# Kernel optimization log

Hardware: AMD Instinct MI355X
Metric: run time of the kernel (lower is better)

The kernel has to match this reference:

```python
import jax, jax.numpy as jnp
import numpy as np

N = 30000
E_RAND = 480000
NFEAT = 512
NHID = 64
NHEADS = 8
NCLASS = 500
ALPHA = 0.2


def setup_inputs() -> dict:
    key = jax.random.key(0)
    ks = jax.random.split(key, 8)
    features = jax.random.normal(ks[0], (N, NFEAT), dtype=jnp.float32)
    src = jax.random.randint(ks[1], (E_RAND,), 0, N, dtype=jnp.int32)
    dst = jax.random.randint(ks[2], (E_RAND,), 0, N, dtype=jnp.int32)
    loop = jnp.arange(N, dtype=jnp.int32)
    edge_index = jnp.stack([jnp.concatenate([src, loop]), jnp.concatenate([dst, loop])])  # [2, E]
    # xavier-normal-ish scaling keeps exp(-leakyrelu(.)) in a sane range
    W = jax.random.normal(ks[3], (NHEADS, NFEAT, NHID), dtype=jnp.float32) * (1.414 * np.sqrt(2.0 / (NFEAT + NHID)))
    a = jax.random.normal(ks[4], (NHEADS, 2 * NHID), dtype=jnp.float32) * (1.414 * np.sqrt(2.0 / (1 + 2 * NHID)))
    out_W = jax.random.normal(ks[5], (NHID * NHEADS, NCLASS), dtype=jnp.float32) * (1.414 * np.sqrt(2.0 / (NHID * NHEADS + NCLASS)))
    out_a = jax.random.normal(ks[6], (2 * NCLASS,), dtype=jnp.float32) * (1.414 * np.sqrt(2.0 / (1 + 2 * NCLASS)))
    return {"features": features, "edge_index": edge_index, "W": W, "a": a, "out_W": out_W, "out_a": out_a}


def _sp_gat_layer(x, W, a, src, dst, concat):
    # h = x @ W  -> [N, F']
    h = x @ W
    f = h.shape[1]
    n = x.shape[0]
    # a . cat(h[src], h[dst]) == (h @ a[:f])[src] + (h @ a[f:])[dst]  (avoids [E, 2F'] concat)
    s_src = h @ a[:f]
    s_dst = h @ a[f:]
    logits = s_src[src] + s_dst[dst]                      # [E]
    edge_e = jnp.exp(-jax.nn.leaky_relu(logits, negative_slope=ALPHA))
    # special_spmm(edge, edge_e, [N,N], ones)  -> per-row sum of attention values
    e_rowsum = jax.ops.segment_sum(edge_e, src, num_segments=n)        # [N]
    # special_spmm(edge, edge_e, [N,N], h)     -> attention-weighted neighbor sum
    h_prime = jax.ops.segment_sum(edge_e[:, None] * h[dst], src, num_segments=n)  # [N, F']
    h_prime = h_prime / e_rowsum[:, None]
    return jax.nn.elu(h_prime) if concat else h_prime


def reference(features, edge_index, W, a, out_W, out_a):
    src, dst = edge_index[0], edge_index[1]
    # multi-head sparse GAT (concat=True per head), python loop over fixed small head count
    heads = [_sp_gat_layer(features, W[i], a[i], src, dst, concat=True) for i in range(W.shape[0])]
    x = jnp.concatenate(heads, axis=1)                    # [N, nhid*nheads]
    out = jax.nn.elu(_sp_gat_layer(x, out_W, out_a, src, dst, concat=False))  # [N, nclass]
    return out
```

## Files before the change

### kernel.cpp

```cpp
#include <hip/hip_runtime.h>
#include <math.h>

typedef __attribute__((ext_vector_type(8))) short short8;
typedef __attribute__((ext_vector_type(4))) float f32x4;

#define NFEAT 512
#define HID_ALL 512
#define NCLASS 500
#define ALPHA 0.2f
#define BM 128
#define BN 128

__device__ __forceinline__ ushort f32_to_bf16(float f) {
    union { float f; unsigned u; } v; v.f = f;
    unsigned u = v.u;
    unsigned r = (u + 0x7FFFu + ((u >> 16) & 1u)) >> 16;
    return (ushort)r;
}
__device__ __forceinline__ void unpack8(uint4 u, float* f) {
    f[0] = __uint_as_float(u.x << 16);
    f[1] = __uint_as_float(u.x & 0xFFFF0000u);
    f[2] = __uint_as_float(u.y << 16);
    f[3] = __uint_as_float(u.y & 0xFFFF0000u);
    f[4] = __uint_as_float(u.z << 16);
    f[5] = __uint_as_float(u.z & 0xFFFF0000u);
    f[6] = __uint_as_float(u.w << 16);
    f[7] = __uint_as_float(u.w & 0xFFFF0000u);
}
__device__ __forceinline__ float att_w(float lg) {
    return __expf(lg > 0.f ? -lg : -ALPHA * lg);
}
__device__ __forceinline__ void gload16(const void* g, void* l) {
    __builtin_amdgcn_global_load_lds(
        (const __attribute__((address_space(1))) unsigned int*)g,
        (__attribute__((address_space(3))) unsigned int*)l,
        16, 0, 0);
}

__global__ void prep_kernel(const float* __restrict__ W, ushort* __restrict__ W1T,
                            const float* __restrict__ oW, ushort* __restrict__ W2T,
                            const float* __restrict__ oa, float* __restrict__ oas,
                            float* __restrict__ oad,
                            int* __restrict__ cnt, int* __restrict__ cur,
                            float* __restrict__ s2, float* __restrict__ d2, int N) {
    int idx = blockIdx.x * blockDim.x + threadIdx.x;
    if (idx < 512 * 512) {
        int c = idx >> 9, f = idx & 511;
        int head = c >> 6, k = c & 63;
        W1T[idx] = f32_to_bf16(W[(head << 15) + (f << 6) + k]);
        float v = (c < NCLASS) ? oW[f * NCLASS + c] : 0.f;
        W2T[idx] = f32_to_bf16(v);
    }
    if (idx < 512) {
        oas[idx] = (idx < NCLASS) ? oa[idx] : 0.f;
        oad[idx] = (idx < NCLASS) ? oa[NCLASS + idx] : 0.f;
    }
    if (idx < N) { cnt[idx] = 0; cur[idx] = 0; s2[idx] = 0.f; d2[idx] = 0.f; }
}

__global__ void cast_feat_kernel(const float* __restrict__ in, ushort* __restrict__ out, int n4) {
    int stride = gridDim.x * blockDim.x;
    for (int i = blockIdx.x * blockDim.x + threadIdx.x; i < n4; i += stride) {
        float4 v = reinterpret_cast<const float4*>(in)[i];
        ushort4 o;
        o.x = f32_to_bf16(v.x); o.y = f32_to_bf16(v.y);
        o.z = f32_to_bf16(v.z); o.w = f32_to_bf16(v.w);
        reinterpret_cast<ushort4*>(out)[i] = o;
    }
}

__global__ void edge_count_kernel(const int* __restrict__ src, int* __restrict__ cnt, int E) {
    int e = blockIdx.x * blockDim.x + threadIdx.x;
    if (e < E) atomicAdd(&cnt[src[e]], 1);
}

__global__ __launch_bounds__(1024) void scan_kernel(const int* __restrict__ cnt,
                                                    int* __restrict__ rowptr, int n) {
    __shared__ int part[1024];
    int t = threadIdx.x;
    int chunk = (n + 1023) >> 10;
    int beg = t * chunk;
    int end = beg + chunk; if (end > n) end = n;
    int s = 0;
    for (int i = beg; i < end; i++) s += cnt[i];
    part[t] = s;
    __syncthreads();
    for (int off = 1; off < 1024; off <<= 1) {
        int v = part[t];
        int add = (t >= off) ? part[t - off] : 0;
        __syncthreads();
        part[t] = v + add;
        __syncthreads();
    }
    int base = (t > 0) ? part[t - 1] : 0;
    for (int i = beg; i < end; i++) { rowptr[i] = base; base += cnt[i]; }
    if (t == 1023) rowptr[n] = part[1023];
}

__global__ void scatter_kernel(const int* __restrict__ src, const int* __restrict__ dst,
                               const int* __restrict__ rowptr, int* __restrict__ cur,
                               int* __restrict__ colidx, int E) {
    int e = blockIdx.x * blockDim.x + threadIdx.x;
    if (e >= E) return;
    int s = src[e];
    int p = rowptr[s] + atomicAdd(&cur[s], 1);
    colidx[p] = dst[e];
}

template <int MODE>
__global__ __launch_bounds__(256) void gemm_fused_kernel(const ushort* __restrict__ A,
                                                         const ushort* __restrict__ Bt,
                                                         ushort* __restrict__ C,
                                                         const float* __restrict__ av,
                                                         const float* __restrict__ av2,
                                                         float* __restrict__ sv,
                                                         float* __restrict__ dv,
                                                         int M) {
    __shared__ ushort As[BM * 64];
    __shared__ ushort Bs[BN * 64];
    int m0 = blockIdx.x * BM;
    int n0 = blockIdx.y * BN;
    int t = threadIdx.x;
    int lane = t & 63, wid = t >> 6;
    int wr = wid >> 1, wc = wid & 1;
    int g = lane >> 4, r15 = lane & 15;
    int srow = lane >> 3;
    int schunk = lane & 7;
    f32x4 acc[4][4] = {};
    for (int k0 = 0; k0 < 512; k0 += 64) {
        __syncthreads();
#pragma unroll
        for (int j = 0; j < 4; j++) {
            int rb = j * 32 + wid * 8;
            int r = rb + srow;
            int ca = (schunk ^ (srow & 7)) << 3;
            int rowA = m0 + r; if (rowA >= M) rowA = M - 1;
            gload16(&A[(size_t)rowA * 512 + k0 + ca], &As[rb * 64]);
            int rowB = n0 + r;
            gload16(&Bt[(size_t)rowB * 512 + k0 + ca], &Bs[rb * 64]);
        }
        __syncthreads();
#pragma unroll
        for (int kk = 0; kk < 2; kk++) {
            int coff = ((kk * 4 + g) ^ (r15 & 7)) << 3;
            short8 af[4], bfr[4];
#pragma unroll
            for (int mi = 0; mi < 4; mi++)
                af[mi] = *reinterpret_cast<const short8*>(&As[((wr << 6) + mi * 16 + r15) * 64 + coff]);
#pragma unroll
            for (int ni = 0; ni < 4; ni++)
                bfr[ni] = *reinterpret_cast<const short8*>(&Bs[((wc << 6) + ni * 16 + r15) * 64 + coff]);
#pragma unroll
            for (int mi = 0; mi < 4; mi++)
#pragma unroll
                for (int ni = 0; ni < 4; ni++)
                    acc[mi][ni] = __builtin_amdgcn_mfma_f32_16x16x32_bf16(af[mi], bfr[ni], acc[mi][ni], 0, 0, 0);
        }
    }
    int fr = g << 2;
    int col = r15;
#pragma unroll
    for (int mi = 0; mi < 4; mi++)
#pragma unroll
        for (int ni = 0; ni < 4; ni++)
#pragma unroll
            for (int r = 0; r < 4; r++) {
                int grow = m0 + (wr << 6) + mi * 16 + fr + r;
                if (grow < M) {
                    int gcol = n0 + (wc << 6) + ni * 16 + col;
                    C[(size_t)grow * 512 + gcol] = f32_to_bf16(acc[mi][ni][r]);
                }
            }
    float ws[4], wd[4];
    int h = (n0 >> 6) + wc;
#pragma unroll
    for (int ni = 0; ni < 4; ni++) {
        if (MODE == 0) {
            int k = ni * 16 + col;
            ws[ni] = av[(h << 7) + k];
            wd[ni] = av[(h << 7) + 64 + k];
        } else {
            int gcol = n0 + (wc << 6) + ni * 16 + col;
            ws[ni] = av[gcol];
            wd[ni] = av2[gcol];
        }
    }
#pragma unroll
    for (int mi = 0; mi < 4; mi++)
#pragma unroll
        for (int r = 0; r < 4; r++) {
            float ps = 0.f, pd = 0.f;
#pragma unroll
            for (int ni = 0; ni < 4; ni++) {
                float v = acc[mi][ni][r];
                ps += v * ws[ni];
                pd += v * wd[ni];
            }
#pragma unroll
            for (int off = 1; off < 16; off <<= 1) {
                ps += __shfl_xor(ps, off);
                pd += __shfl_xor(pd, off);
            }
            int grow = m0 + (wr << 6) + mi * 16 + fr + r;
            if (col == 0 && grow < M) {
                if (MODE == 0) {
                    sv[(grow << 3) + h] = ps;
                    dv[(grow << 3) + h] = pd;
                } else {
                    atomicAdd(&sv[grow], ps);
                    atomicAdd(&dv[grow], pd);
                }
            }
        }
}

__global__ __launch_bounds__(256) void agg1_kernel(const ushort* __restrict__ h1,
                                                   const float* __restrict__ s1,
                                                   const float* __restrict__ d1,
                                                   const int* __restrict__ rowptr,
                                                   const int* __restrict__ colidx,
                                                   ushort* __restrict__ x, int N) {
    int lane = threadIdx.x & 63;
    int n = (blockIdx.x << 2) + (threadIdx.x >> 6);
    if (n >= N) return;
    int h = lane >> 3;
    float sn = s1[(n << 3) + h];
    float acc[8] = {0.f, 0.f, 0.f, 0.f, 0.f, 0.f, 0.f, 0.f};
    float rsum = 0.f;
    int beg = rowptr[n], end = rowptr[n + 1];
    int i = beg;
    for (; i + 4 <= end; i += 4) {
        int dv0 = colidx[i], dv1 = colidx[i + 1], dv2 = colidx[i + 2], dv3 = colidx[i + 3];
        float g0 = d1[(dv0 << 3) + h];
        float g1 = d1[(dv1 << 3) + h];
        float g2 = d1[(dv2 << 3) + h];
        float g3 = d1[(dv3 << 3) + h];
        uint4 u0 = *reinterpret_cast<const uint4*>(&h1[(size_t)dv0 * 512 + lane * 8]);
        uint4 u1 = *reinterpret_cast<const uint4*>(&h1[(size_t)dv1 * 512 + lane * 8]);
        uint4 u2 = *reinterpret_cast<const uint4*>(&h1[(size_t)dv2 * 512 + lane * 8]);
        uint4 u3 = *reinterpret_cast<const uint4*>(&h1[(size_t)dv3 * 512 + lane * 8]);
        float w0 = att_w(sn + g0), w1 = att_w(sn + g1), w2 = att_w(sn + g2), w3 = att_w(sn + g3);
        rsum += (w0 + w1) + (w2 + w3);
        float f[8];
        unpack8(u0, f);
#pragma unroll
        for (int q = 0; q < 8; q++) acc[q] += w0 * f[q];
        unpack8(u1, f);
#pragma unroll
        for (int q = 0; q < 8; q++) acc[q] += w1 * f[q];
        unpack8(u2, f);
#pragma unroll
        for (int q = 0; q < 8; q++) acc[q] += w2 * f[q];
        unpack8(u3, f);
#pragma unroll
        for (int q = 0; q < 8; q++) acc[q] += w3 * f[q];
    }
    for (; i < end; i++) {
        int dv = colidx[i];
        float w = att_w(sn + d1[(dv << 3) + h]);
        rsum += w;
        uint4 u = *reinterpret_cast<const uint4*>(&h1[(size_t)dv * 512 + lane * 8]);
        float f[8]; unpack8(u, f);
#pragma unroll
        for (int q = 0; q < 8; q++) acc[q] += w * f[q];
    }
    float inv = 1.f / rsum;
    uint ov[4];
#pragma unroll
    for (int p = 0; p < 4; p++) {
        float v0 = acc[2 * p] * inv;     v0 = v0 > 0.f ? v0 : __expf(v0) - 1.f;
        float v1 = acc[2 * p + 1] * inv; v1 = v1 > 0.f ? v1 : __expf(v1) - 1.f;
        ov[p] = (uint)f32_to_bf16(v0) | ((uint)f32_to_bf16(v1) << 16);
    }
    uint4 o; o.x = ov[0]; o.y = ov[1]; o.z = ov[2]; o.w = ov[3];
    *reinterpret_cast<uint4*>(&x[(size_t)n * 512 + lane * 8]) = o;
}

__global__ __launch_bounds__(256) void agg2_kernel(const ushort* __restrict__ h2,
                                                   const float* __restrict__ s2,
                                                   const float* __restrict__ d2,
                                                   const int* __restrict__ rowptr,
                                                   const int* __restrict__ colidx,
                                                   float* __restrict__ out, int N) {
    int lane = threadIdx.x & 63;
    int n = (blockIdx.x << 2) + (threadIdx.x >> 6);
    if (n >= N) return;
    int c0 = lane * 8;
    float sn = s2[n];
    float acc[8] = {0.f, 0.f, 0.f, 0.f, 0.f, 0.f, 0.f, 0.f};
    float rsum = 0.f;
    int beg = rowptr[n], end = rowptr[n + 1];
    int i = beg;
    for (; i + 4 <= end; i += 4) {
        int dv0 = colidx[i], dv1 = colidx[i + 1], dv2 = colidx[i + 2], dv3 = colidx[i + 3];
        float g0 = d2[dv0], g1 = d2[dv1], g2 = d2[dv2], g3 = d2[dv3];
        uint4 u0 = *reinterpret_cast<const uint4*>(&h2[(size_t)dv0 * 512 + c0]);
        uint4 u1 = *reinterpret_cast<const uint4*>(&h2[(size_t)dv1 * 512 + c0]);
        uint4 u2 = *reinterpret_cast<const uint4*>(&h2[(size_t)dv2 * 512 + c0]);
        uint4 u3 = *reinterpret_cast<const uint4*>(&h2[(size_t)dv3 * 512 + c0]);
        float w0 = att_w(sn + g0), w1 = att_w(sn + g1), w2 = att_w(sn + g2), w3 = att_w(sn + g3);
        rsum += (w0 + w1) + (w2 + w3);
        float f[8];
        unpack8(u0, f);
#pragma unroll
        for (int q = 0; q < 8; q++) acc[q] += w0 * f[q];
        unpack8(u1, f);
#pragma unroll
        for (int q = 0; q < 8; q++) acc[q] += w1 * f[q];
        unpack8(u2, f);
#pragma unroll
        for (int q = 0; q < 8; q++) acc[q] += w2 * f[q];
        unpack8(u3, f);
#pragma unroll
        for (int q = 0; q < 8; q++) acc[q] += w3 * f[q];
    }
    for (; i < end; i++) {
        int dv = colidx[i];
        float w = att_w(sn + d2[dv]);
        rsum += w;
        uint4 u = *reinterpret_cast<const uint4*>(&h2[(size_t)dv * 512 + c0]);
        float f[8]; unpack8(u, f);
#pragma unroll
        for (int q = 0; q < 8; q++) acc[q] += w * f[q];
    }
    float inv = 1.f / rsum;
#pragma unroll
    for (int q = 0; q < 8; q++) {
        int c = c0 + q;
        if (c < NCLASS) {
            float v = acc[q] * inv;
            v = v > 0.f ? v : __expf(v) - 1.f;
            out[(size_t)n * NCLASS + c] = v;
        }
    }
}

extern "C" void kernel_launch(void* const* d_in, const int* in_sizes, int n_in,
                              void* d_out, int out_size, void* d_ws, size_t ws_size,
                              hipStream_t stream) {
    const float* features = (const float*)d_in[0];
    const int* edge_index = (const int*)d_in[1];
    const float* W = (const float*)d_in[2];
    const float* a = (const float*)d_in[3];
    const float* out_W = (const float*)d_in[4];
    const float* out_a = (const float*)d_in[5];
    float* out = (float*)d_out;

    int N = in_sizes[0] / NFEAT;
    int E = in_sizes[1] / 2;
    const int* src = edge_index;
    const int* dst = edge_index + E;

    char* base = (char*)d_ws;
    size_t off = 0;
    auto alloc = [&](size_t bytes) -> char* {
        char* r = base + off;
        off += (bytes + 255) & ~(size_t)255;
        return r;
    };
    ushort* featb = (ushort*)alloc((size_t)N * 512 * 2);
    ushort* h1b   = (ushort*)alloc((size_t)N * 512 * 2);
    ushort* xb    = (ushort*)alloc((size_t)N * 512 * 2);
    ushort* h2b   = featb;
    ushort* w1t   = (ushort*)alloc(512 * 512 * 2);
    ushort* w2t   = (ushort*)alloc(512 * 512 * 2);
    float* s1 = (float*)alloc((size_t)N * 8 * 4);
    float* d1 = (float*)alloc((size_t)N * 8 * 4);
    float* s2 = (float*)alloc((size_t)N * 4);
    float* d2 = (float*)alloc((size_t)N * 4);
    float* oas = (float*)alloc(512 * 4);
    float* oad = (float*)alloc(512 * 4);
    int* rowptr = (int*)alloc((size_t)(N + 1) * 4);
    int* colidx = (int*)alloc((size_t)E * 4);
    int* cnt = (int*)alloc((size_t)N * 4);
    int* cur = (int*)alloc((size_t)N * 4);
    if (off > ws_size) return;

    prep_kernel<<<1024, 256, 0, stream>>>(W, w1t, out_W, w2t, out_a, oas, oad, cnt, cur, s2, d2, N);
    cast_feat_kernel<<<2048, 256, 0, stream>>>(features, featb, N * 512 / 4);
    edge_count_kernel<<<(E + 255) / 256, 256, 0, stream>>>(src, cnt, E);
    scan_kernel<<<1, 1024, 0, stream>>>(cnt, rowptr, N);
    scatter_kernel<<<(E + 255) / 256, 256, 0, stream>>>(src, dst, rowptr, cur, colidx, E);

    dim3 gemm_grid((N + BM - 1) / BM, HID_ALL / BN);
    gemm_fused_kernel<0><<<gemm_grid, 256, 0, stream>>>(featb, w1t, h1b, a, nullptr, s1, d1, N);
    agg1_kernel<<<(N + 3) / 4, 256, 0, stream>>>(h1b, s1, d1, rowptr, colidx, xb, N);
    gemm_fused_kernel<1><<<gemm_grid, 256, 0, stream>>>(xb, w2t, h2b, oas, oad, s2, d2, N);
    agg2_kernel<<<(N + 3) / 4, 256, 0, stream>>>(h2b, s2, d2, rowptr, colidx, out, N);
}
```

Measured before the change: 342.2 us.

## Transpose weights via shared-memory tiles and read GEMM B operand from global

Weight transposition and bf16 casting move out of the strided prep kernel into two tiled shared-memory transpose kernels, so both reads and writes are coalesced. The GEMM also stops staging the B (weight) tile in LDS and loads B fragments straight from global memory, relying on L2/L1 caching of the small weight matrix. This halves LDS use per block, which may raise occupancy, but it exposes global-load latency inside the MFMA inner loop with no prefetching.

```diff
diff --git a/kernel.cpp b/kernel.cpp
--- a/kernel.cpp
+++ b/kernel.cpp
@@ -37,25 +37,56 @@
         16, 0, 0);
 }
 
-__global__ void prep_kernel(const float* __restrict__ W, ushort* __restrict__ W1T,
-                            const float* __restrict__ oW, ushort* __restrict__ W2T,
-                            const float* __restrict__ oa, float* __restrict__ oas,
+__global__ void prep_kernel(const float* __restrict__ oa, float* __restrict__ oas,
                             float* __restrict__ oad,
                             int* __restrict__ cnt, int* __restrict__ cur,
                             float* __restrict__ s2, float* __restrict__ d2, int N) {
     int idx = blockIdx.x * blockDim.x + threadIdx.x;
-    if (idx < 512 * 512) {
-        int c = idx >> 9, f = idx & 511;
-        int head = c >> 6, k = c & 63;
-        W1T[idx] = f32_to_bf16(W[(head << 15) + (f << 6) + k]);
-        float v = (c < NCLASS) ? oW[f * NCLASS + c] : 0.f;
-        W2T[idx] = f32_to_bf16(v);
-    }
     if (idx < 512) {
         oas[idx] = (idx < NCLASS) ? oa[idx] : 0.f;
         oad[idx] = (idx < NCLASS) ? oa[NCLASS + idx] : 0.f;
     }
     if (idx < N) { cnt[idx] = 0; cur[idx] = 0; s2[idx] = 0.f; d2[idx] = 0.f; }
+}
+
+__global__ __launch_bounds__(256) void transpose_w1_kernel(const float* __restrict__ W,
+                                                           ushort* __restrict__ WT) {
+    __shared__ float tile[64][65];
+    int head = blockIdx.x >> 3;
+    int f0 = (blockIdx.x & 7) << 6;
+    int tx = threadIdx.x & 63, tyb = threadIdx.x >> 6;
+    const float* Wh = W + ((size_t)head << 15);
+#pragma unroll
+    for (int r = 0; r < 16; r++) {
+        int ty = (tyb << 4) + r;
+        tile[ty][tx] = Wh[(size_t)(f0 + ty) * 64 + tx];
+    }
+    __syncthreads();
+#pragma unroll
+    for (int r = 0; r < 16; r++) {
+        int ty = (tyb << 4) + r;
+        WT[(size_t)((head << 6) + ty) * 512 + f0 + tx] = f32_to_bf16(tile[tx][ty]);
+    }
+}
+
+__global__ __launch_bounds__(256) void transpose_w2_kernel(const float* __restrict__ oW,
+                                                           ushort* __restrict__ WT) {
+    __shared__ float tile[64][65];
+    int f0 = (blockIdx.x >> 3) << 6;
+    int c0 = (blockIdx.x & 7) << 6;
+    int tx = threadIdx.x & 63, tyb = threadIdx.x >> 6;
+#pragma unroll
+    for (int r = 0; r < 16; r++) {
+        int ty = (tyb << 4) + r;
+        int c = c0 + tx;
+        tile[ty][tx] = (c < NCLASS) ? oW[(size_t)(f0 + ty) * NCLASS + c] : 0.f;
+    }
+    __syncthreads();
+#pragma unroll
+    for (int r = 0; r < 16; r++) {
+        int ty = (tyb << 4) + r;
+        WT[(size_t)(c0 + ty) * 512 + f0 + tx] = f32_to_bf16(tile[tx][ty]);
+    }
 }
 
 __global__ void cast_feat_kernel(const float* __restrict__ in, ushort* __restrict__ out, int n4) {
@@ -117,7 +148,6 @@
                                                          float* __restrict__ dv,
                                                          int M) {
     __shared__ ushort As[BM * 64];
-    __shared__ ushort Bs[BN * 64];
     int m0 = blockIdx.x * BM;
     int n0 = blockIdx.y * BN;
     int t = threadIdx.x;
@@ -136,8 +166,6 @@
             int ca = (schunk ^ (srow & 7)) << 3;
             int rowA = m0 + r; if (rowA >= M) rowA = M - 1;
             gload16(&A[(size_t)rowA * 512 + k0 + ca], &As[rb * 64]);
-            int rowB = n0 + r;
-            gload16(&Bt[(size_t)rowB * 512 + k0 + ca], &Bs[rb * 64]);
         }
         __syncthreads();
 #pragma unroll
@@ -149,7 +177,8 @@
                 af[mi] = *reinterpret_cast<const short8*>(&As[((wr << 6) + mi * 16 + r15) * 64 + coff]);
 #pragma unroll
             for (int ni = 0; ni < 4; ni++)
-                bfr[ni] = *reinterpret_cast<const short8*>(&Bs[((wc << 6) + ni * 16 + r15) * 64 + coff]);
+                bfr[ni] = *reinterpret_cast<const short8*>(
+                    &Bt[(size_t)(n0 + (wc << 6) + ni * 16 + r15) * 512 + k0 + kk * 32 + g * 8]);
 #pragma unroll
             for (int mi = 0; mi < 4; mi++)
 #pragma unroll
@@ -376,7 +405,9 @@
     int* cur = (int*)alloc((size_t)N * 4);
     if (off > ws_size) return;
 
-    prep_kernel<<<1024, 256, 0, stream>>>(W, w1t, out_W, w2t, out_a, oas, oad, cnt, cur, s2, d2, N);
+    prep_kernel<<<(N + 255) / 256, 256, 0, stream>>>(out_a, oas, oad, cnt, cur, s2, d2, N);
+    transpose_w1_kernel<<<64, 256, 0, stream>>>(W, w1t);
+    transpose_w2_kernel<<<64, 256, 0, stream>>>(out_W, w2t);
     cast_feat_kernel<<<2048, 256, 0, stream>>>(features, featb, N * 512 / 4);
     edge_count_kernel<<<(E + 255) / 256, 256, 0, stream>>>(src, cnt, E);
     scan_kernel<<<1, 1024, 0, stream>>>(cnt, rowptr, N);
```

Measured after the change: 381.3 us. 1.11x slower.
